# Kernel optimization log

Measured on AMD Instinct MI355X. Metric: run time of the kernel, lower is better.

The kernel has to match this reference:

```python
import jax, jax.numpy as jnp
import numpy as np


def sparsemax(z):
    # Sparsemax along last axis: Euclidean projection of z onto the simplex.
    S = z.shape[-1]
    z_sorted = jnp.flip(jnp.sort(z, axis=-1), axis=-1)          # descending
    cssv = jnp.cumsum(z_sorted, axis=-1)                         # cumulative sums
    r = jnp.arange(1, S + 1, dtype=z.dtype)                      # 1..S
    support = 1.0 + r * z_sorted > cssv                          # support mask
    k = jnp.sum(support, axis=-1, keepdims=True)                 # support size (int)
    tau = (jnp.take_along_axis(cssv, k - 1, axis=-1) - 1.0) / k.astype(z.dtype)
    return jnp.maximum(z - tau, 0.0)


def setup_inputs() -> dict:
    key = jax.random.key(0)
    k1, k2, k3 = jax.random.split(key, 3)
    B, L, S, H, E, D = 8, 1024, 1024, 16, 64, 64
    queries = jax.random.normal(k1, (B, L, H, E), dtype=jnp.float32)
    keys = jax.random.normal(k2, (B, S, H, E), dtype=jnp.float32)
    values = jax.random.normal(k3, (B, S, H, D), dtype=jnp.float32)
    return {"queries": queries, "keys": keys, "values": values}


def reference(queries, keys, values):
    E = queries.shape[-1]
    scale = 1.0 / jnp.sqrt(jnp.asarray(E, dtype=queries.dtype))
    # [B,H,L,S] attention scores
    scores = jnp.einsum('blhe,bshe->bhls', queries, keys)
    A = sparsemax(scale * scores)                                # sparsemax normalization (dropout p=0)
    attn_output = jnp.einsum('bhls,bshd->blhd', A, values)
    return attn_output
```

## Files before the change

### kernel.cpp

```cpp
#include <hip/hip_runtime.h>


typedef _Float16 f16x8 __attribute__((ext_vector_type(8)));
typedef float    f32x4 __attribute__((ext_vector_type(4)));

constexpr int kB = 8, kL = 1024, kS = 1024, kH = 16, kE = 64, kD = 64;
constexpr int LT   = 32;
constexpr int JT   = 128;
constexpr int CAP  = 192;
constexpr int KMAX = CAP / 16;

__device__ __forceinline__ float pk2(float a, float b) {
  auto h = __builtin_amdgcn_cvt_pkrtz(a, b);
  return __builtin_bit_cast(float, h);
}

__global__ __launch_bounds__(512, 4)
void sparsemax_attn(const float* __restrict__ Q, const float* __restrict__ K,
                    const float* __restrict__ V, float* __restrict__ O) {
  __shared__ float4 Ksh[JT * 8];
  __shared__ float4 Qsh[LT * 8];
  __shared__ float2 lists[LT * CAP];
  __shared__ int    cnt_s[LT];
  __shared__ float  rmax_s[LT][4];
  __shared__ float  tau_s[LT];

  const int t = threadIdx.x, lane = t & 63, w = t >> 6;
  const int qg = w >> 2, jg = w & 3;
  const int li = lane & 15, g = lane >> 4;
  const int myrow = qg * 16 + li;

  const int id  = blockIdx.x;
  const int xcd = id & 7, kk = id >> 3;
  const int bh  = xcd * 16 + (kk >> 5);
  const int b   = bh >> 4, h = bh & 15;
  const int l0  = (kk & 31) * LT;

  const float* Kbh = K + ((size_t)b * kS * kH + h) * kE;
  const float* Vb  = V + ((size_t)b * kS * kH + h) * kD;

  if (t < LT) cnt_s[t] = 0;
  if (t < 256) {
    const int jj = t >> 3, e8 = t & 7;
    const float4* qp =
        (const float4*)(Q + (((size_t)(b * kL + l0 + jj)) * kH + h) * kE + e8 * 8);
    float4 q0 = qp[0], q1 = qp[1];
    q0.x *= .125f; q0.y *= .125f; q0.z *= .125f; q0.w *= .125f;
    q1.x *= .125f; q1.y *= .125f; q1.z *= .125f; q1.w *= .125f;
    Qsh[jj * 8 + (e8 ^ (jj & 7))] =
        make_float4(pk2(q0.x, q0.y), pk2(q0.z, q0.w), pk2(q1.x, q1.y), pk2(q1.z, q1.w));
  }

  float runl = -1e30f;
  f16x8 b0, b1;

  for (int jt = 0; jt < kS / JT; ++jt) {
    __syncthreads();
#pragma unroll
    for (int i = 0; i < 2; ++i) {
      const int idx = t + 512 * i, jj = idx >> 3, e8 = idx & 7;
      const float4* kp =
          (const float4*)(Kbh + (size_t)(jt * JT + jj) * (kH * kE) + e8 * 8);
      const float4 c0 = kp[0], c1 = kp[1];
      Ksh[jj * 8 + (e8 ^ (jj & 7))] =
          make_float4(pk2(c0.x, c0.y), pk2(c0.z, c0.w), pk2(c1.x, c1.y), pk2(c1.z, c1.w));
    }
    __syncthreads();
    if (jt == 0) {
      b0 = __builtin_bit_cast(f16x8, Qsh[myrow * 8 + ((0 + g) ^ (myrow & 7))]);
      b1 = __builtin_bit_cast(f16x8, Qsh[myrow * 8 + ((4 + g) ^ (myrow & 7))]);
    }

    f32x4 acc[2];
    acc[0] = f32x4{0.f, 0.f, 0.f, 0.f};
    acc[1] = f32x4{0.f, 0.f, 0.f, 0.f};
#pragma unroll
    for (int ct = 0; ct < 2; ++ct) {
      const int jl = jg * 32 + ct * 16 + li;
      const f16x8 a0 = __builtin_bit_cast(f16x8, Ksh[jl * 8 + ((0 + g) ^ (jl & 7))]);
      const f16x8 a1 = __builtin_bit_cast(f16x8, Ksh[jl * 8 + ((4 + g) ^ (jl & 7))]);
      acc[ct] = __builtin_amdgcn_mfma_f32_16x16x32_f16(a0, b0, acc[ct], 0, 0, 0);
      acc[ct] = __builtin_amdgcn_mfma_f32_16x16x32_f16(a1, b1, acc[ct], 0, 0, 0);
    }

    const float m01 = fmaxf(fmaxf(acc[0][0], acc[0][1]), fmaxf(acc[0][2], acc[0][3]));
    const float m23 = fmaxf(fmaxf(acc[1][0], acc[1][1]), fmaxf(acc[1][2], acc[1][3]));
    runl = fmaxf(runl, fmaxf(m01, m23));
    float mr = fmaxf(runl, __shfl_xor(runl, 16));
    mr = fmaxf(mr, __shfl_xor(mr, 32));
    const float thr = mr - 1.0f;
    const int jbase = jt * JT + jg * 32 + g * 4;
#pragma unroll
    for (int ct = 0; ct < 2; ++ct)
#pragma unroll
      for (int r = 0; r < 4; ++r) {
        const float z = acc[ct][r];
        if (z > thr) {
          const int pos = atomicAdd(&cnt_s[myrow], 1);
          if (pos < CAP)
            lists[myrow * CAP + pos] =
                make_float2(z, __int_as_float(jbase + ct * 16 + r));
        }
      }
  }
  {
    float mr = fmaxf(runl, __shfl_xor(runl, 16));
    mr = fmaxf(mr, __shfl_xor(mr, 32));
    if (lane < 16) rmax_s[myrow][jg] = mr;
  }
  __syncthreads();

  const int q0 = w * 4;
  {
    const int row = q0 + g;
    const int n   = cnt_s[row];
    const int nc  = min(n, CAP);
    float zr[KMAX];
#pragma unroll
    for (int k = 0; k < KMAX; ++k) {
      const int i = li + 16 * k;
      zr[k] = (i < nc) ? lists[row * CAP + i].x : -1e30f;
    }
    const float M =
        fmaxf(fmaxf(rmax_s[row][0], rmax_s[row][1]), fmaxf(rmax_s[row][2], rmax_s[row][3]));
    float t0 = M - 1.0f;
    for (int it = 0; it < 14; ++it) {
      float s = 0.f, c = 0.f;
#pragma unroll
      for (int k = 0; k < KMAX; ++k) {
        const float d = zr[k] - t0;
        if (d > 0.f) { s += d; c += 1.f; }
      }
      s += __shfl_xor(s, 1); c += __shfl_xor(c, 1);
      s += __shfl_xor(s, 2); c += __shfl_xor(c, 2);
      s += __shfl_xor(s, 4); c += __shfl_xor(c, 4);
      s += __shfl_xor(s, 8); c += __shfl_xor(c, 8);
      const float delta = (s - 1.0f) / fmaxf(c, 1.f);
      t0 += fmaxf(delta, 0.f);
      if (__all(delta <= 1e-6f)) break;
    }
    if (li == 0) tau_s[row] = t0;
  }

#pragma unroll 1
  for (int r4 = 0; r4 < 4; ++r4) {
    const int row = q0 + r4;
    const int n   = cnt_s[row];
    const size_t obase = (((size_t)(b * kL + l0 + row)) * kH + h) * kD;
    if (n <= CAP) {
      const float tau = tau_s[row];
      f32x4 o4 = {0.f, 0.f, 0.f, 0.f};
      for (int i = g; i < n; i += 4) {
        const float2 e = lists[row * CAP + i];
        const float  p = fmaxf(e.x - tau, 0.f);
        const float4 v =
            ((const float4*)(Vb + (size_t)__float_as_int(e.y) * (kH * kD)))[li];
        o4.x = fmaf(p, v.x, o4.x);
        o4.y = fmaf(p, v.y, o4.y);
        o4.z = fmaf(p, v.z, o4.z);
        o4.w = fmaf(p, v.w, o4.w);
      }
      o4.x += __shfl_xor(o4.x, 16); o4.y += __shfl_xor(o4.y, 16);
      o4.z += __shfl_xor(o4.z, 16); o4.w += __shfl_xor(o4.w, 16);
      o4.x += __shfl_xor(o4.x, 32); o4.y += __shfl_xor(o4.y, 32);
      o4.z += __shfl_xor(o4.z, 32); o4.w += __shfl_xor(o4.w, 32);
      if (lane < 16)
        ((float4*)(O + obase))[li] = make_float4(o4.x, o4.y, o4.z, o4.w);
    } else {
      float scr2[16];
      for (int cc = 0; cc < 16; ++cc) {
        const int j = lane + 64 * cc;
        const float* kr = Kbh + (size_t)j * (kH * kE);
        float zz = 0.f;
        for (int e8 = 0; e8 < 8; ++e8) {
          const f16x8 qh = __builtin_bit_cast(f16x8, Qsh[row * 8 + (e8 ^ (row & 7))]);
          const float4* kp = (const float4*)(kr + e8 * 8);
          const float4 c0 = kp[0], c1 = kp[1];
          zz += (float)qh[0] * c0.x + (float)qh[1] * c0.y + (float)qh[2] * c0.z +
                (float)qh[3] * c0.w + (float)qh[4] * c1.x + (float)qh[5] * c1.y +
                (float)qh[6] * c1.z + (float)qh[7] * c1.w;
        }
        scr2[cc] = zz;
      }
      const float M2 =
          fmaxf(fmaxf(rmax_s[row][0], rmax_s[row][1]), fmaxf(rmax_s[row][2], rmax_s[row][3]));
      float t0 = M2 - 1.0f;
      for (int it = 0; it < 48; ++it) {
        float s = 0.f, c = 0.f;
        for (int cc = 0; cc < 16; ++cc) {
          const float d = scr2[cc] - t0;
          if (d > 0.f) { s += d; c += 1.f; }
        }
        for (int off = 32; off; off >>= 1) { s += __shfl_xor(s, off); c += __shfl_xor(c, off); }
        const float delta = (s - 1.0f) / fmaxf(c, 1.f);
        if (delta <= 1e-7f) break;
        t0 += delta;
      }
      float oacc = 0.f;
      for (int cc = 0; cc < 16; ++cc)
        for (int src = 0; src < 64; ++src) {
          const float z = __shfl(scr2[cc], src);
          const float p = z - t0;
          if (p > 0.f)
            oacc = fmaf(p, Vb[(size_t)(src + 64 * cc) * (kH * kD) + lane], oacc);
        }
      O[obase + lane] = oacc;
    }
  }
}

extern "C" void kernel_launch(void* const* d_in, const int* in_sizes, int n_in,
                              void* d_out, int out_size, void* d_ws, size_t ws_size,
                              hipStream_t stream) {
  (void)in_sizes; (void)n_in; (void)out_size; (void)d_ws; (void)ws_size;
  const float* Q = (const float*)d_in[0];
  const float* K = (const float*)d_in[1];
  const float* V = (const float*)d_in[2];
  float* O = (float*)d_out;
  sparsemax_attn<<<dim3(kB * kH * (kL / LT)), dim3(512), 0, stream>>>(Q, K, V, O);
}
```

Before: 498.9 us.

## Load K fragments directly from global memory, drop K LDS staging and barriers

Removes the shared-memory K tile and the two per-tile block barriers; each lane now loads its K row fragment straight from global memory, converts it to fp16 and feeds the MFMA. This frees LDS and allows a higher occupancy hint (6 blocks per CU). The sparse PV gather loop is also unrolled by two so that more V loads are in flight at once. The trade-off is that K rows are no longer shared across waves, so the same K data is re-read from global memory or cache by each query group with less coalesced access.

```diff
diff --git a/kernel.cpp b/kernel.cpp
--- a/kernel.cpp
+++ b/kernel.cpp
@@ -15,10 +15,16 @@
   return __builtin_bit_cast(float, h);
 }
 
-__global__ __launch_bounds__(512, 4)
+__device__ __forceinline__ f16x8 ldk8(const float* __restrict__ p) {
+  const float4 c0 = ((const float4*)p)[0], c1 = ((const float4*)p)[1];
+  const float4 r = make_float4(pk2(c0.x, c0.y), pk2(c0.z, c0.w),
+                               pk2(c1.x, c1.y), pk2(c1.z, c1.w));
+  return __builtin_bit_cast(f16x8, r);
+}
+
+__global__ __launch_bounds__(512, 6)
 void sparsemax_attn(const float* __restrict__ Q, const float* __restrict__ K,
                     const float* __restrict__ V, float* __restrict__ O) {
-  __shared__ float4 Ksh[JT * 8];
   __shared__ float4 Qsh[LT * 8];
   __shared__ float2 lists[LT * CAP];
   __shared__ int    cnt_s[LT];
@@ -50,35 +56,26 @@
     Qsh[jj * 8 + (e8 ^ (jj & 7))] =
         make_float4(pk2(q0.x, q0.y), pk2(q0.z, q0.w), pk2(q1.x, q1.y), pk2(q1.z, q1.w));
   }
+  __syncthreads();
+
+  const f16x8 b0 = __builtin_bit_cast(f16x8, Qsh[myrow * 8 + ((0 + g) ^ (myrow & 7))]);
+  const f16x8 b1 = __builtin_bit_cast(f16x8, Qsh[myrow * 8 + ((4 + g) ^ (myrow & 7))]);
+
+  const float* Klane = Kbh + (size_t)(jg * 32 + li) * (kH * kE) + g * 8;
 
   float runl = -1e30f;
-  f16x8 b0, b1;
 
   for (int jt = 0; jt < kS / JT; ++jt) {
-    __syncthreads();
-#pragma unroll
-    for (int i = 0; i < 2; ++i) {
-      const int idx = t + 512 * i, jj = idx >> 3, e8 = idx & 7;
-      const float4* kp =
-          (const float4*)(Kbh + (size_t)(jt * JT + jj) * (kH * kE) + e8 * 8);
-      const float4 c0 = kp[0], c1 = kp[1];
-      Ksh[jj * 8 + (e8 ^ (jj & 7))] =
-          make_float4(pk2(c0.x, c0.y), pk2(c0.z, c0.w), pk2(c1.x, c1.y), pk2(c1.z, c1.w));
-    }
-    __syncthreads();
-    if (jt == 0) {
-      b0 = __builtin_bit_cast(f16x8, Qsh[myrow * 8 + ((0 + g) ^ (myrow & 7))]);
-      b1 = __builtin_bit_cast(f16x8, Qsh[myrow * 8 + ((4 + g) ^ (myrow & 7))]);
-    }
+    const float* kt = Klane + (size_t)jt * JT * (kH * kE);
 
     f32x4 acc[2];
     acc[0] = f32x4{0.f, 0.f, 0.f, 0.f};
     acc[1] = f32x4{0.f, 0.f, 0.f, 0.f};
 #pragma unroll
     for (int ct = 0; ct < 2; ++ct) {
-      const int jl = jg * 32 + ct * 16 + li;
-      const f16x8 a0 = __builtin_bit_cast(f16x8, Ksh[jl * 8 + ((0 + g) ^ (jl & 7))]);
-      const f16x8 a1 = __builtin_bit_cast(f16x8, Ksh[jl * 8 + ((4 + g) ^ (jl & 7))]);
+      const float* kr = kt + (size_t)ct * 16 * (kH * kE);
+      const f16x8 a0 = ldk8(kr);
+      const f16x8 a1 = ldk8(kr + 32);
       acc[ct] = __builtin_amdgcn_mfma_f32_16x16x32_f16(a0, b0, acc[ct], 0, 0, 0);
       acc[ct] = __builtin_amdgcn_mfma_f32_16x16x32_f16(a1, b1, acc[ct], 0, 0, 0);
     }
@@ -149,16 +146,23 @@
     const size_t obase = (((size_t)(b * kL + l0 + row)) * kH + h) * kD;
     if (n <= CAP) {
       const float tau = tau_s[row];
+      const int nc = n;
       f32x4 o4 = {0.f, 0.f, 0.f, 0.f};
-      for (int i = g; i < n; i += 4) {
-        const float2 e = lists[row * CAP + i];
-        const float  p = fmaxf(e.x - tau, 0.f);
-        const float4 v =
-            ((const float4*)(Vb + (size_t)__float_as_int(e.y) * (kH * kD)))[li];
-        o4.x = fmaf(p, v.x, o4.x);
-        o4.y = fmaf(p, v.y, o4.y);
-        o4.z = fmaf(p, v.z, o4.z);
-        o4.w = fmaf(p, v.w, o4.w);
+      for (int i = g; i < nc; i += 8) {
+        const int   i2 = i + 4;
+        const bool  ok2 = (i2 < nc);
+        const float2 e1 = lists[row * CAP + i];
+        const float2 e2 = lists[row * CAP + (ok2 ? i2 : i)];
+        const float  p1 = fmaxf(e1.x - tau, 0.f);
+        const float  p2 = ok2 ? fmaxf(e2.x - tau, 0.f) : 0.f;
+        const float4 v1 =
+            ((const float4*)(Vb + (size_t)__float_as_int(e1.y) * (kH * kD)))[li];
+        const float4 v2 =
+            ((const float4*)(Vb + (size_t)__float_as_int(e2.y) * (kH * kD)))[li];
+        o4.x = fmaf(p1, v1.x, fmaf(p2, v2.x, o4.x));
+        o4.y = fmaf(p1, v1.y, fmaf(p2, v2.y, o4.y));
+        o4.z = fmaf(p1, v1.z, fmaf(p2, v2.z, o4.z));
+        o4.w = fmaf(p1, v1.w, fmaf(p2, v2.w, o4.w));
       }
       o4.x += __shfl_xor(o4.x, 16); o4.y += __shfl_xor(o4.y, 16);
       o4.z += __shfl_xor(o4.z, 16); o4.w += __shfl_xor(o4.w, 16);
```

Result: slower. 729.1 us (+46.1%).
